# Kernel optimization log

Hardware: AMD Instinct MI355X
Metric: run time of the kernel (lower is better)

The kernel has to match this reference:

```python
import jax, jax.numpy as jnp
import numpy as np

B, H, HKV, S, D = 2, 32, 8, 2048, 64
SCALE = 0.125  # 1/sqrt(D)
EPS = 1e-9     # kernel divides by (l + 1e-9)


def setup_inputs() -> dict:
    key = jax.random.key(0)
    kq, kk, kv = jax.random.split(key, 3)
    Q = jax.random.normal(kq, (B, H, S, D), dtype=jnp.float32)
    K = jax.random.normal(kk, (B, HKV, S, D), dtype=jnp.float32)
    V = jax.random.normal(kv, (B, HKV, S, D), dtype=jnp.float32)
    return {"Q": Q, "K": K, "V": V}


def reference(Q, K, V):
    # Grouped-query attention with KV-head sharing, non-causal, full softmax.
    b, h, s, d = Q.shape
    hkv = K.shape[1]
    g = h // hkv  # query heads per kv head; h = kvh*g + gi (contiguous groups)
    Qg = Q.reshape(b, hkv, g, s, d)
    # scores: [b, hkv, g, s_q, s_k]
    scores = jnp.einsum("bkgsd,bktd->bkgst", Qg, K) * SCALE
    m = jnp.max(scores, axis=-1, keepdims=True)
    p = jnp.exp(scores - m)
    l = jnp.sum(p, axis=-1, keepdims=True)  # [b,hkv,g,s,1]
    out = jnp.einsum("bkgst,bktd->bkgsd", p, V) / (l + EPS)
    return out.reshape(b, h, s, d)
```

## Files before the change

### kernel.cpp

```cpp
#include <hip/hip_runtime.h>

#define NB 2
#define NH 32
#define NKV 8
#define SEQ 2048
#define DH 64
#define TQ 256
#define TK 64

typedef _Float16 f16x4 __attribute__((ext_vector_type(4)));
typedef _Float16 f16x8 __attribute__((ext_vector_type(8)));
typedef float f32x4 __attribute__((ext_vector_type(4)));

#define MFMA(A, B, C) __builtin_amdgcn_mfma_f32_16x16x32_f16(A, B, C, 0, 0, 0)

__device__ __forceinline__ int swz(int row, int hcol) {
  return (row << 6) + ((((hcol >> 3) ^ (row & 7)) << 3) | (hcol & 7));
}

__global__ __launch_bounds__(256) void gqa_fused(
    const float* __restrict__ Qg, const float* __restrict__ Kg,
    const float* __restrict__ Vg, float* __restrict__ Og) {
  __shared__ _Float16 Kt[2][TK * DH];
  __shared__ _Float16 Vt[2][DH * TK];
  __shared__ _Float16 Pt[TQ * TK];

  const int tid  = threadIdx.x;
  const int wave = tid >> 6;
  const int lane = tid & 63;
  const int quad = lane >> 4;
  const int l16  = lane & 15;

  const int qt  = blockIdx.x;
  const int hq  = blockIdx.y;
  const int b   = blockIdx.z;
  const int hkv = hq >> 2;

  const float* Qb = Qg + (((size_t)b * NH + hq) * SEQ + (size_t)qt * TQ) * DH;
  const float* Kb = Kg + ((size_t)b * NKV + hkv) * (size_t)SEQ * DH;
  const float* Vb = Vg + ((size_t)b * NKV + hkv) * (size_t)SEQ * DH;
  float* Ob       = Og + (((size_t)b * NH + hq) * SEQ + (size_t)qt * TQ) * DH;

  const float qscale = 0.125f * 1.44269504088896341f;

  f16x8 aQ[4][2];
#pragma unroll
  for (int sl = 0; sl < 4; ++sl) {
    const float* qp = Qb + (size_t)(wave * 64 + sl * 16 + l16) * DH + quad * 8;
#pragma unroll
    for (int c = 0; c < 2; ++c) {
      const float4 f0 = *reinterpret_cast<const float4*>(qp + c * 32);
      const float4 f1 = *reinterpret_cast<const float4*>(qp + c * 32 + 4);
      union { f16x8 v; _Float16 e[8]; } u;
      u.e[0] = (_Float16)(f0.x * qscale);
      u.e[1] = (_Float16)(f0.y * qscale);
      u.e[2] = (_Float16)(f0.z * qscale);
      u.e[3] = (_Float16)(f0.w * qscale);
      u.e[4] = (_Float16)(f1.x * qscale);
      u.e[5] = (_Float16)(f1.y * qscale);
      u.e[6] = (_Float16)(f1.z * qscale);
      u.e[7] = (_Float16)(f1.w * qscale);
      aQ[sl][c] = u.v;
    }
  }

  f32x4 o[4][4], lp[4];
#pragma unroll
  for (int sl = 0; sl < 4; ++sl) {
    lp[sl] = (f32x4){0.f, 0.f, 0.f, 0.f};
#pragma unroll
    for (int n = 0; n < 4; ++n) o[sl][n] = (f32x4){0.f, 0.f, 0.f, 0.f};
  }

  const int kkey = tid >> 3;
  const int kd8  = (tid & 7) << 3;
  float4 kpre[2][2];
  float vpre[2][8];
  auto load_tile = [&](int kt) {
#pragma unroll
    for (int it = 0; it < 2; ++it) {
      const float* kp = Kb + (size_t)(kt + it * 32 + kkey) * DH + kd8;
      kpre[it][0] = *reinterpret_cast<const float4*>(kp);
      kpre[it][1] = *reinterpret_cast<const float4*>(kp + 4);
    }
#pragma unroll
    for (int ao = 0; ao < 2; ++ao) {
      const int a = wave + 4 * ao;
      const float* vp = Vb + (size_t)(kt + 2 * a) * DH + lane;
#pragma unroll
      for (int t = 0; t < 4; ++t) {
        vpre[ao][t]     = vp[(size_t)(16 * t) * DH];
        vpre[ao][t + 4] = vp[(size_t)(16 * t + 1) * DH];
      }
    }
  };

  auto stage_tile = [&](int buf) {
#pragma unroll
    for (int it = 0; it < 2; ++it) {
      union { f16x8 v; _Float16 e[8]; } u;
      u.e[0] = (_Float16)kpre[it][0].x;
      u.e[1] = (_Float16)kpre[it][0].y;
      u.e[2] = (_Float16)kpre[it][0].z;
      u.e[3] = (_Float16)kpre[it][0].w;
      u.e[4] = (_Float16)kpre[it][1].x;
      u.e[5] = (_Float16)kpre[it][1].y;
      u.e[6] = (_Float16)kpre[it][1].z;
      u.e[7] = (_Float16)kpre[it][1].w;
      *reinterpret_cast<f16x8*>(&Kt[buf][swz(it * 32 + kkey, kd8)]) = u.v;
    }
#pragma unroll
    for (int ao = 0; ao < 2; ++ao) {
      union { f16x8 v; _Float16 e[8]; } u;
#pragma unroll
      for (int j = 0; j < 8; ++j) u.e[j] = (_Float16)vpre[ao][j];
      *reinterpret_cast<f16x8*>(&Vt[buf][swz(lane, 8 * (wave + 4 * ao))]) = u.v;
    }
  };

  load_tile(0);
  stage_tile(0);
  __syncthreads();

  for (int kt = 0; kt < SEQ; kt += TK) {
    const int cur   = (kt >> 6) & 1;
    const bool more = (kt + TK) < SEQ;

    f16x8 bK[4][2];
#pragma unroll
    for (int n = 0; n < 4; ++n)
#pragma unroll
      for (int c = 0; c < 2; ++c)
        bK[n][c] = *reinterpret_cast<const f16x8*>(
            &Kt[cur][swz(n * 16 + l16, c * 32 + quad * 8)]);

#pragma unroll
    for (int sl = 0; sl < 4; ++sl) {
      f32x4 s[4];
#pragma unroll
      for (int n = 0; n < 4; ++n) {
        f32x4 acc = (f32x4){0.f, 0.f, 0.f, 0.f};
        acc = MFMA(aQ[sl][0], bK[n][0], acc);
        acc = MFMA(aQ[sl][1], bK[n][1], acc);
        s[n] = acc;
      }
      const int prow = wave * 64 + sl * 16 + quad * 4;
#pragma unroll
      for (int r = 0; r < 4; ++r) {
        union { f16x4 v; _Float16 e[4]; } u;
        float lacc = 0.f;
#pragma unroll
        for (int n = 0; n < 4; ++n) {
          const float e = __builtin_amdgcn_exp2f(s[n][r]);
          lacc += e;
          u.e[n] = (_Float16)e;
        }
        lp[sl][r] += lacc;
        *reinterpret_cast<f16x4*>(&Pt[swz(prow + r, l16 << 2)]) = u.v;
      }
      if (sl == 1 && more) load_tile(kt + TK);
    }
    __asm__ volatile("s_waitcnt lgkmcnt(0)" ::: "memory");

    f16x8 aP[4][2], bV[4][2];
#pragma unroll
    for (int sl = 0; sl < 4; ++sl)
#pragma unroll
      for (int c = 0; c < 2; ++c)
        aP[sl][c] = *reinterpret_cast<const f16x8*>(
            &Pt[swz(wave * 64 + sl * 16 + l16, c * 32 + quad * 8)]);
#pragma unroll
    for (int n = 0; n < 4; ++n)
#pragma unroll
      for (int c = 0; c < 2; ++c)
        bV[n][c] = *reinterpret_cast<const f16x8*>(
            &Vt[cur][swz(n * 16 + l16, c * 32 + quad * 8)]);

#pragma unroll
    for (int sl = 0; sl < 4; ++sl)
#pragma unroll
      for (int n = 0; n < 4; ++n) {
        o[sl][n] = MFMA(aP[sl][0], bV[n][0], o[sl][n]);
        o[sl][n] = MFMA(aP[sl][1], bV[n][1], o[sl][n]);
      }

    if (more) stage_tile(cur ^ 1);
    __syncthreads();
  }

#pragma unroll
  for (int sl = 0; sl < 4; ++sl)
#pragma unroll
    for (int r = 0; r < 4; ++r) {
      float sum = lp[sl][r];
      sum += __shfl_xor(sum, 1);
      sum += __shfl_xor(sum, 2);
      sum += __shfl_xor(sum, 4);
      sum += __shfl_xor(sum, 8);
      const float inv = 1.f / (sum + 1e-9f);
      const size_t row = (size_t)(wave * 64 + sl * 16 + quad * 4 + r);
#pragma unroll
      for (int n = 0; n < 4; ++n)
        Ob[row * DH + n * 16 + l16] = o[sl][n][r] * inv;
    }
}

extern "C" void kernel_launch(void* const* d_in, const int* in_sizes, int n_in,
                              void* d_out, int out_size, void* d_ws, size_t ws_size,
                              hipStream_t stream) {
  const float* Q = (const float*)d_in[0];
  const float* K = (const float*)d_in[1];
  const float* V = (const float*)d_in[2];
  float* O = (float*)d_out;
  dim3 grid(SEQ / TQ, NH, NB);
  gqa_fused<<<grid, 256, 0, stream>>>(Q, K, V, O);
}
```

Baseline: 196.1 us.

## Single-buffer K/V LDS tiles, convert prefetch to fp16 early, raise occupancy hint

Replaces the double-buffered K/V shared-memory tiles with single buffers and adds a second barrier per iteration. The register prefetch of the next tile is now converted to fp16 at load time and issued right after staging, instead of partway through the softmax loop. All QK^T MFMAs are grouped before the exp pass, and launch bounds ask for two blocks per CU. This cuts LDS and register use to allow more resident blocks, at the cost of an extra barrier and possible register pressure from holding the 16 score accumulators.

```diff
diff --git a/kernel.cpp b/kernel.cpp
--- a/kernel.cpp
+++ b/kernel.cpp
@@ -18,11 +18,11 @@
   return (row << 6) + ((((hcol >> 3) ^ (row & 7)) << 3) | (hcol & 7));
 }
 
-__global__ __launch_bounds__(256) void gqa_fused(
+__global__ __launch_bounds__(256, 2) void gqa_fused(
     const float* __restrict__ Qg, const float* __restrict__ Kg,
     const float* __restrict__ Vg, float* __restrict__ Og) {
-  __shared__ _Float16 Kt[2][TK * DH];
-  __shared__ _Float16 Vt[2][DH * TK];
+  __shared__ _Float16 Kt[TK * DH];
+  __shared__ _Float16 Vt[DH * TK];
   __shared__ _Float16 Pt[TQ * TK];
 
   const int tid  = threadIdx.x;
@@ -74,57 +74,53 @@
 
   const int kkey = tid >> 3;
   const int kd8  = (tid & 7) << 3;
-  float4 kpre[2][2];
-  float vpre[2][8];
+  f16x8 kh[2];
+  f16x8 vh[2];
   auto load_tile = [&](int kt) {
 #pragma unroll
     for (int it = 0; it < 2; ++it) {
       const float* kp = Kb + (size_t)(kt + it * 32 + kkey) * DH + kd8;
-      kpre[it][0] = *reinterpret_cast<const float4*>(kp);
-      kpre[it][1] = *reinterpret_cast<const float4*>(kp + 4);
+      const float4 f0 = *reinterpret_cast<const float4*>(kp);
+      const float4 f1 = *reinterpret_cast<const float4*>(kp + 4);
+      union { f16x8 v; _Float16 e[8]; } u;
+      u.e[0] = (_Float16)f0.x;
+      u.e[1] = (_Float16)f0.y;
+      u.e[2] = (_Float16)f0.z;
+      u.e[3] = (_Float16)f0.w;
+      u.e[4] = (_Float16)f1.x;
+      u.e[5] = (_Float16)f1.y;
+      u.e[6] = (_Float16)f1.z;
+      u.e[7] = (_Float16)f1.w;
+      kh[it] = u.v;
     }
 #pragma unroll
     for (int ao = 0; ao < 2; ++ao) {
       const int a = wave + 4 * ao;
       const float* vp = Vb + (size_t)(kt + 2 * a) * DH + lane;
+      union { f16x8 v; _Float16 e[8]; } u;
 #pragma unroll
       for (int t = 0; t < 4; ++t) {
-        vpre[ao][t]     = vp[(size_t)(16 * t) * DH];
-        vpre[ao][t + 4] = vp[(size_t)(16 * t + 1) * DH];
-      }
+        u.e[t]     = (_Float16)vp[(size_t)(16 * t) * DH];
+        u.e[t + 4] = (_Float16)vp[(size_t)(16 * t + 1) * DH];
+      }
+      vh[ao] = u.v;
     }
   };
 
-  auto stage_tile = [&](int buf) {
-#pragma unroll
-    for (int it = 0; it < 2; ++it) {
-      union { f16x8 v; _Float16 e[8]; } u;
-      u.e[0] = (_Float16)kpre[it][0].x;
-      u.e[1] = (_Float16)kpre[it][0].y;
-      u.e[2] = (_Float16)kpre[it][0].z;
-      u.e[3] = (_Float16)kpre[it][0].w;
-      u.e[4] = (_Float16)kpre[it][1].x;
-      u.e[5] = (_Float16)kpre[it][1].y;
-      u.e[6] = (_Float16)kpre[it][1].z;
-      u.e[7] = (_Float16)kpre[it][1].w;
-      *reinterpret_cast<f16x8*>(&Kt[buf][swz(it * 32 + kkey, kd8)]) = u.v;
-    }
-#pragma unroll
-    for (int ao = 0; ao < 2; ++ao) {
-      union { f16x8 v; _Float16 e[8]; } u;
-#pragma unroll
-      for (int j = 0; j < 8; ++j) u.e[j] = (_Float16)vpre[ao][j];
-      *reinterpret_cast<f16x8*>(&Vt[buf][swz(lane, 8 * (wave + 4 * ao))]) = u.v;
-    }
-  };
-
   load_tile(0);
-  stage_tile(0);
-  __syncthreads();
 
   for (int kt = 0; kt < SEQ; kt += TK) {
-    const int cur   = (kt >> 6) & 1;
-    const bool more = (kt + TK) < SEQ;
+    __syncthreads();
+
+#pragma unroll
+    for (int it = 0; it < 2; ++it)
+      *reinterpret_cast<f16x8*>(&Kt[swz(it * 32 + kkey, kd8)]) = kh[it];
+#pragma unroll
+    for (int ao = 0; ao < 2; ++ao)
+      *reinterpret_cast<f16x8*>(&Vt[swz(lane, 8 * (wave + 4 * ao))]) = vh[ao];
+    __syncthreads();
+
+    if (kt + TK < SEQ) load_tile(kt + TK);
 
     f16x8 bK[4][2];
 #pragma unroll
@@ -132,18 +128,21 @@
 #pragma unroll
       for (int c = 0; c < 2; ++c)
         bK[n][c] = *reinterpret_cast<const f16x8*>(
-            &Kt[cur][swz(n * 16 + l16, c * 32 + quad * 8)]);
-
-#pragma unroll
-    for (int sl = 0; sl < 4; ++sl) {
-      f32x4 s[4];
+            &Kt[swz(n * 16 + l16, c * 32 + quad * 8)]);
+
+    f32x4 s[4][4];
+#pragma unroll
+    for (int sl = 0; sl < 4; ++sl)
 #pragma unroll
       for (int n = 0; n < 4; ++n) {
         f32x4 acc = (f32x4){0.f, 0.f, 0.f, 0.f};
         acc = MFMA(aQ[sl][0], bK[n][0], acc);
         acc = MFMA(aQ[sl][1], bK[n][1], acc);
-        s[n] = acc;
-      }
+        s[sl][n] = acc;
+      }
+
+#pragma unroll
+    for (int sl = 0; sl < 4; ++sl) {
       const int prow = wave * 64 + sl * 16 + quad * 4;
 #pragma unroll
       for (int r = 0; r < 4; ++r) {
@@ -151,14 +150,13 @@
         float lacc = 0.f;
 #pragma unroll
         for (int n = 0; n < 4; ++n) {
-          const float e = __builtin_amdgcn_exp2f(s[n][r]);
+          const float e = __builtin_amdgcn_exp2f(s[sl][n][r]);
           lacc += e;
           u.e[n] = (_Float16)e;
         }
         lp[sl][r] += lacc;
         *reinterpret_cast<f16x4*>(&Pt[swz(prow + r, l16 << 2)]) = u.v;
       }
-      if (sl == 1 && more) load_tile(kt + TK);
     }
     __asm__ volatile("s_waitcnt lgkmcnt(0)" ::: "memory");
 
@@ -174,7 +172,7 @@
 #pragma unroll
       for (int c = 0; c < 2; ++c)
         bV[n][c] = *reinterpret_cast<const f16x8*>(
-            &Vt[cur][swz(n * 16 + l16, c * 32 + quad * 8)]);
+            &Vt[swz(n * 16 + l16, c * 32 + quad * 8)]);
 
 #pragma unroll
     for (int sl = 0; sl < 4; ++sl)
@@ -183,9 +181,6 @@
         o[sl][n] = MFMA(aP[sl][0], bV[n][0], o[sl][n]);
         o[sl][n] = MFMA(aP[sl][1], bV[n][1], o[sl][n]);
       }
-
-    if (more) stage_tile(cur ^ 1);
-    __syncthreads();
   }
 
 #pragma unroll
```

After: 176.8 us. 9.9% less time.
